# Optimization experiments

Hardware: AMD Instinct MI355X
Metric: run time of the kernel (lower is better)

Reference implementation:

```python
import jax, jax.numpy as jnp
import numpy as np

B, L, H, E = 8, 1024, 8, 64
S = 1024
T = 1.0


def setup_inputs() -> dict:
    key = jax.random.key(0)
    kq, kk, kv = jax.random.split(key, 3)
    q = jax.random.normal(kq, (B, L, H, E), dtype=jnp.float32)
    k = jax.random.normal(kk, (B, S, H, E), dtype=jnp.float32)
    v = jax.random.normal(kv, (B, S, H, E), dtype=jnp.float32)
    attn_mask = jnp.zeros((1,), dtype=bool)  # unused by the module
    return {"q": q, "k": k, "v": v, "attn_mask": attn_mask}


def reference(q, k, v, attn_mask):
    # q: [B,L,H,E], k/v: [B,S,H,E]; attn_mask unused (matches torch source)
    Bq, Lq, Hq, Eq = q.shape
    xq = jnp.transpose(q, (0, 2, 3, 1))  # [B,H,E,L]
    xk = jnp.transpose(k, (0, 2, 3, 1))  # [B,H,E,S]
    xv = jnp.transpose(v, (0, 2, 3, 1))  # [B,H,E,S]
    qf = jnp.fft.rfft(xq, axis=-1, norm="ortho")  # [B,H,E,Lf]
    kf = jnp.fft.rfft(xk, axis=-1, norm="ortho")  # [B,H,E,Sf]
    vf = jnp.fft.rfft(xv, axis=-1, norm="ortho")  # [B,H,E,Sf]
    # complex cross-frequency scores, contracted over head dim E
    scores = jnp.einsum("bhex,bhey->bhxy", qf, jnp.conj(kf)) / jnp.sqrt(
        jnp.float32(Eq)
    )  # [B,H,Lf,Sf] complex
    # magnitude softmax -> real weights, promoted back to complex (zero imag)
    attn = jax.nn.softmax(jnp.abs(scores) / jnp.float32(T), axis=-1)
    attn = attn.astype(scores.dtype)
    outf = jnp.einsum("bhxy,bhey->bhex", attn, vf)  # [B,H,E,Lf] complex
    out = jnp.fft.irfft(outf, n=Lq, axis=-1, norm="ortho")  # [B,H,E,L] real
    return jnp.transpose(out, (0, 3, 1, 2))  # [B,L,H,E]
```

## Files before the change

### kernel.cpp

```cpp
#include <hip/hip_runtime.h>
#include <hip/hip_fp16.h>
#include <math.h>

#define BATCH 8
#define LSEQ  1024
#define NH    8
#define EDIM  64
#define LF    513
#define NBH   64
#define YP    576

typedef _Float16 f16;
typedef _Float16 f16x8 __attribute__((ext_vector_type(8)));
typedef float    f32x4 __attribute__((ext_vector_type(4)));
typedef unsigned int u32x4 __attribute__((ext_vector_type(4)));

__device__ __forceinline__ float2 cadd(float2 a, float2 b){return make_float2(a.x+b.x, a.y+b.y);}
__device__ __forceinline__ float2 csub(float2 a, float2 b){return make_float2(a.x-b.x, a.y-b.y);}
__device__ __forceinline__ float2 cmuls(float2 w, float2 y, float sign){
  float wr = w.x, wi = sign * w.y;
  return make_float2(y.x*wr - y.y*wi, y.x*wi + y.y*wr);
}

template<int ST>
__device__ __forceinline__ void r4stage(const float2* S, float2* D,
                                        const float2* __restrict__ tw,
                                        int bt, float sign) {
  const int s = 1 << (2*ST);
  const int q = bt & (s - 1);
  const int j1 = bt - q;
  float2 a0 = S[bt], a1 = S[bt+256], a2 = S[bt+512], a3 = S[bt+768];
  float2 b0 = cadd(a0,a2), b1 = csub(a0,a2);
  float2 b2 = cadd(a1,a3), b3 = csub(a1,a3);
  float2 y0 = cadd(b0,b2), y2 = csub(b0,b2);
  float2 ib3 = make_float2(-sign*b3.y, sign*b3.x);
  float2 y1 = cadd(b1, ib3), y3 = csub(b1, ib3);
  const int wb = 4*bt - 3*q;
  D[wb]       = y0;
  D[wb +   s] = cmuls(tw[j1],   y1, sign);
  D[wb + 2*s] = cmuls(tw[2*j1], y2, sign);
  D[wb + 3*s] = cmuls(tw[3*j1], y3, sign);
}

__device__ __forceinline__ void fft1024x2_r4(float2* fb0, float2* fb1,
                                             const float2* __restrict__ tw,
                                             int t, float sign) {
  const int off = (t >> 8) << 10;
  const int bt  = t & 255;
  r4stage<0>(fb0+off, fb1+off, tw, bt, sign); __syncthreads();
  r4stage<1>(fb1+off, fb0+off, tw, bt, sign); __syncthreads();
  r4stage<2>(fb0+off, fb1+off, tw, bt, sign); __syncthreads();
  r4stage<3>(fb1+off, fb0+off, tw, bt, sign); __syncthreads();
  r4stage<4>(fb0+off, fb1+off, tw, bt, sign); __syncthreads();
}

__global__ __launch_bounds__(512) void rfft_pack_kernel(
    const float* __restrict__ q, const float* __restrict__ k, const float* __restrict__ v,
    f16* __restrict__ qf, f16* __restrict__ kf, f16* __restrict__ vfT) {
  __shared__ float2 fb0[2048];
  __shared__ float2 fb1[2048];
  __shared__ float2 tw[768];
  const int t = threadIdx.x;
  const int equad = blockIdx.x;
  const int bh = blockIdx.y;
  const int tensor = blockIdx.z;
  const int b = bh >> 3, h = bh & 7;
  const int e0 = equad * 4;
  const float* src = (tensor == 0) ? q : ((tensor == 1) ? k : v);

  for (int i = t; i < 768; i += 512) {
    float sv, cv;
    __sincosf(6.2831853071795864769f * (float)i * (1.0f / 1024.0f), &sv, &cv);
    tw[i] = make_float2(cv, sv);
  }
  #pragma unroll
  for (int i = 0; i < 2; i++) {
    int l = t + i * 512;
    float4 vv = *(const float4*)(src + (((size_t)b * LSEQ + l) * NH + h) * EDIM + e0);
    fb0[l]        = make_float2(vv.x, vv.y);
    fb0[1024 + l] = make_float2(vv.z, vv.w);
  }
  __syncthreads();
  fft1024x2_r4(fb0, fb1, tw, t, -1.0f);

  #pragma unroll
  for (int i = 0; i < 2; i++) {
    int kk = t + i * 512;
    if (kk <= 512) {
      const float sc = 0.015625f;
      if (tensor < 2) {
        union { f16 hh[8]; u32x4 u; } pk;
        #pragma unroll
        for (int f = 0; f < 2; f++) {
          float2 z  = fb1[(f << 10) + kk];
          float2 zn = fb1[(f << 10) + ((1024 - kk) & 1023)];
          pk.hh[f*4+0] = (f16)(sc * (z.x + zn.x));
          pk.hh[f*4+1] = (f16)(sc * (z.y - zn.y));
          pk.hh[f*4+2] = (f16)(sc * (z.y + zn.y));
          pk.hh[f*4+3] = (f16)(sc * (zn.x - z.x));
        }
        f16* dst = (tensor == 0) ? qf : kf;
        *(u32x4*)(dst + ((size_t)bh * YP + kk) * 128 + e0 * 2) = pk.u;
      } else {
        #pragma unroll
        for (int f = 0; f < 2; f++) {
          float2 z  = fb1[(f << 10) + kk];
          float2 zn = fb1[(f << 10) + ((1024 - kk) & 1023)];
          size_t base = (size_t)bh * 128 + e0 * 2 + f * 4;
          vfT[(base + 0) * YP + kk] = (f16)(sc * (z.x + zn.x));
          vfT[(base + 1) * YP + kk] = (f16)(sc * (z.y - zn.y));
          vfT[(base + 2) * YP + kk] = (f16)(sc * (z.y + zn.y));
          vfT[(base + 3) * YP + kk] = (f16)(sc * (zn.x - z.x));
        }
      }
    }
  }
  if (tensor == 2 && t < 63) {
    int kk = 513 + t;
    #pragma unroll
    for (int j = 0; j < 8; j++)
      vfT[((size_t)bh * 128 + e0 * 2 + j) * YP + kk] = (f16)0.0f;
  }
}

__device__ __forceinline__ int pmidx(int row, int y) {
  return row * YP + (y ^ ((row & 7) << 3));
}

__global__ __launch_bounds__(256, 4) void fused_attn_kernel(
    const f16* __restrict__ qf, const f16* __restrict__ kf,
    const f16* __restrict__ vfT, float* __restrict__ of) {
  __shared__ f16 pm[32 * YP];
  __shared__ float winv_s[32];
  const int tid = threadIdx.x;
  const int w = tid >> 6, l = tid & 63, lr = l & 15, lg = l >> 4;
  const int bh = blockIdx.y, x0 = blockIdx.x * 32;
  const int xsub = w & 1, yhalf = w >> 1;

  for (int i = tid; i < 2048; i += 256) {
    int row = i >> 6, yo = i & 63;
    if (yo) pm[pmidx(row, 512 + yo)] = (f16)0.0f;
  }

  const f16* qb = qf + ((size_t)bh * YP + x0 + xsub * 16 + lr) * 128 + lg * 8;
  f16x8 aq[4], aqs[4];
  #pragma unroll
  for (int c4 = 0; c4 < 4; c4++) {
    aq[c4] = *(const f16x8*)(qb + c4 * 32);
    u32x4 tt = *(const u32x4*)&aq[c4];
    u32x4 ss;
    #pragma unroll
    for (int d = 0; d < 4; d++)
      ss[d] = ((tt[d] >> 16) | (tt[d] << 16)) ^ 0x80000000u;
    aqs[c4] = *(const f16x8*)&ss;
  }

  const int ntile = yhalf ? 15 : 18;
  const f16* kb = kf + ((size_t)bh * YP + yhalf * 288 + lr) * 128 + lg * 8;

  f16x8 kA[4], kB[4];
  #pragma unroll
  for (int c4 = 0; c4 < 4; c4++) kA[c4] = *(const f16x8*)(kb + c4 * 32);

#define PROCA(KR, TT) {                                                        \
    f32x4 rr = {0.f,0.f,0.f,0.f}, ri = {0.f,0.f,0.f,0.f};                      \
    _Pragma("unroll")                                                          \
    for (int c4 = 0; c4 < 4; c4++) {                                           \
      rr = __builtin_amdgcn_mfma_f32_16x16x32_f16(aq[c4],  KR[c4], rr, 0,0,0); \
      ri = __builtin_amdgcn_mfma_f32_16x16x32_f16(aqs[c4], KR[c4], ri, 0,0,0); \
    }                                                                          \
    int y = yhalf * 288 + (TT) * 16 + lr;                                      \
    if (y <= 512) {                                                            \
      int rowb = xsub * 16 + lg * 4;                                           \
      _Pragma("unroll")                                                        \
      for (int i = 0; i < 4; i++)                                              \
        pm[pmidx(rowb + i, y)] = (f16)(0.125f * sqrtf(rr[i]*rr[i] + ri[i]*ri[i])); \
    }                                                                          \
  }

  for (int t = 0; t < ntile; t += 2) {
    if (t + 1 < ntile) {
      const f16* kp = kb + (size_t)(t + 1) * 2048;
      #pragma unroll
      for (int c4 = 0; c4 < 4; c4++) kB[c4] = *(const f16x8*)(kp + c4 * 32);
    }
    PROCA(kA, t)
    if (t + 1 < ntile) {
      if (t + 2 < ntile) {
        const f16* kp = kb + (size_t)(t + 2) * 2048;
        #pragma unroll
        for (int c4 = 0; c4 < 4; c4++) kA[c4] = *(const f16x8*)(kp + c4 * 32);
      }
      PROCA(kB, t + 1)
    }
  }
#undef PROCA
  __syncthreads();

  #pragma unroll 1
  for (int r = 0; r < 8; r++) {
    const int row = w * 8 + r;
    float mx = 0.0f;
    #pragma unroll
    for (int ps = 0; ps < 4; ps++) {
      __half2 hv = *(const __half2*)&pm[pmidx(row, 2 * (l + 64 * ps))];
      float2 f = __half22float2(hv);
      mx = fmaxf(mx, fmaxf(f.x, f.y));
    }
    if (l < 32) {
      __half2 hv = *(const __half2*)&pm[pmidx(row, 512 + 2 * l)];
      float2 f = __half22float2(hv);
      mx = fmaxf(mx, fmaxf(f.x, f.y));
    }
    #pragma unroll
    for (int o = 32; o > 0; o >>= 1) mx = fmaxf(mx, __shfl_xor(mx, o));

    float s = 0.0f;
    #pragma unroll
    for (int ps = 0; ps < 4; ps++) {
      int y = 2 * (l + 64 * ps);
      __half2 hv = *(const __half2*)&pm[pmidx(row, y)];
      float2 f = __half22float2(hv);
      float p0 = __expf(f.x - mx), p1 = __expf(f.y - mx);
      s += p0 + p1;
      *(__half2*)&pm[pmidx(row, y)] = __floats2half2_rn(p0, p1);
    }
    if (l < 32) {
      int y = 512 + 2 * l;
      __half2 hv = *(const __half2*)&pm[pmidx(row, y)];
      float2 f = __half22float2(hv);
      float p0 = (y <= 512) ? __expf(f.x - mx) : 0.0f;
      s += p0;
      *(__half2*)&pm[pmidx(row, y)] = __floats2half2_rn(p0, 0.0f);
    }
    #pragma unroll
    for (int o = 32; o > 0; o >>= 1) s += __shfl_xor(s, o);
    if (l == 0) winv_s[row] = 1.0f / s;
  }
  __syncthreads();

  const int ch = (w >> 1) * 64;
  f32x4 acc[4];
  #pragma unroll
  for (int nt = 0; nt < 4; nt++) acc[nt] = (f32x4){0.f,0.f,0.f,0.f};
  const f16* vb = vfT + ((size_t)bh * 128 + ch + lr) * YP + lg * 8;

  f16x8 vA[4], vB[4];
  #pragma unroll
  for (int nt = 0; nt < 4; nt++) vA[nt] = *(const f16x8*)(vb + (size_t)(nt * 16) * YP);

  for (int kc = 0; kc < 18; kc += 2) {
    #pragma unroll
    for (int nt = 0; nt < 4; nt++)
      vB[nt] = *(const f16x8*)(vb + (size_t)(nt * 16) * YP + (kc + 1) * 32);
    {
      f16x8 a = *(const f16x8*)&pm[pmidx(xsub * 16 + lr, kc * 32 + lg * 8)];
      #pragma unroll
      for (int nt = 0; nt < 4; nt++)
        acc[nt] = __builtin_amdgcn_mfma_f32_16x16x32_f16(a, vA[nt], acc[nt], 0, 0, 0);
    }
    if (kc + 2 < 18) {
      #pragma unroll
      for (int nt = 0; nt < 4; nt++)
        vA[nt] = *(const f16x8*)(vb + (size_t)(nt * 16) * YP + (kc + 2) * 32);
    }
    {
      f16x8 a = *(const f16x8*)&pm[pmidx(xsub * 16 + lr, (kc + 1) * 32 + lg * 8)];
      #pragma unroll
      for (int nt = 0; nt < 4; nt++)
        acc[nt] = __builtin_amdgcn_mfma_f32_16x16x32_f16(a, vB[nt], acc[nt], 0, 0, 0);
    }
  }
  #pragma unroll
  for (int i = 0; i < 4; i++) {
    int xl = xsub * 16 + lg * 4 + i;
    int x = x0 + xl;
    if (x < LF) {
      float wv = winv_s[xl];
      #pragma unroll
      for (int nt = 0; nt < 4; nt++)
        of[((size_t)bh * LF + x) * 128 + ch + nt * 16 + lr] = acc[nt][i] * wv;
    }
  }
}

__global__ __launch_bounds__(512) void irfft_kernel(
    const float* __restrict__ of, float* __restrict__ out) {
  __shared__ float2 fb0[2048];
  __shared__ float2 fb1[2048];
  __shared__ float2 tw[768];
  const int t = threadIdx.x;
  const int equad = blockIdx.x;
  const int bh = blockIdx.y;
  const int b = bh >> 3, h = bh & 7;
  const int e0 = equad * 4;

  for (int i = t; i < 768; i += 512) {
    float sv, cv;
    __sincosf(6.2831853071795864769f * (float)i * (1.0f / 1024.0f), &sv, &cv);
    tw[i] = make_float2(cv, sv);
  }
  #pragma unroll
  for (int i = 0; i < 2; i++) {
    int kk = t + i * 512;
    if (kk <= 512) {
      const float* pr = of + ((size_t)bh * LF + kk) * 128 + e0 * 2;
      float4 r0 = *(const float4*)pr;
      float4 r1 = *(const float4*)(pr + 4);
      fb0[kk]        = make_float2(r0.x - r0.w, r0.y + r0.z);
      fb0[1024 + kk] = make_float2(r1.x - r1.w, r1.y + r1.z);
      if (kk >= 1 && kk <= 511) {
        fb0[1024 - kk]        = make_float2(r0.x + r0.w, r0.z - r0.y);
        fb0[1024 + 1024 - kk] = make_float2(r1.x + r1.w, r1.z - r1.y);
      }
    }
  }
  __syncthreads();
  fft1024x2_r4(fb0, fb1, tw, t, +1.0f);
  #pragma unroll
  for (int i = 0; i < 2; i++) {
    int l = t + i * 512;
    float2 z0 = fb1[l], z1 = fb1[1024 + l];
    float4 o = make_float4(0.03125f * z0.x, 0.03125f * z0.y,
                           0.03125f * z1.x, 0.03125f * z1.y);
    *(float4*)(out + (((size_t)b * LSEQ + l) * NH + h) * EDIM + e0) = o;
  }
}

extern "C" void kernel_launch(void* const* d_in, const int* in_sizes, int n_in,
                              void* d_out, int out_size, void* d_ws, size_t ws_size,
                              hipStream_t stream) {
  const float* q = (const float*)d_in[0];
  const float* k = (const float*)d_in[1];
  const float* v = (const float*)d_in[2];
  float* out = (float*)d_out;
  char* ws = (char*)d_ws;

  f16*   qf  = (f16*)(ws);
  f16*   kf  = (f16*)(ws + 9437184);
  f16*   vfT = (f16*)(ws + 18874368);
  float* of  = (float*)(ws + 28311552);

  rfft_pack_kernel<<<dim3(16, NBH, 3), 512, 0, stream>>>(q, k, v, qf, kf, vfT);
  fused_attn_kernel<<<dim3(17, NBH), 256, 0, stream>>>(qf, kf, vfT, of);
  irfft_kernel<<<dim3(16, NBH), 512, 0, stream>>>(of, out);
}
```

Baseline: 262.5 us.

## Swizzle FFT shared-memory indices and shrink attention tile to 16 query rows

Applies an XOR swizzle to every shared-memory index in the radix-4 FFT stages of the forward and inverse FFT kernels, to reduce LDS bank conflicts from strided butterfly accesses. The fused attention kernel now handles 16 frequency rows per block instead of 32. The four waves split the key range four ways for the score computation and the 128 output channels four ways for the value product. This halves LDS use and doubles the grid size for more occupancy, but each K/V tile is reused across fewer query rows, raising global traffic, and the explicit register double-buffering of loads is removed.

```diff
diff --git a/kernel.cpp b/kernel.cpp
--- a/kernel.cpp
+++ b/kernel.cpp
@@ -21,6 +21,7 @@
   float wr = w.x, wi = sign * w.y;
   return make_float2(y.x*wr - y.y*wi, y.x*wi + y.y*wr);
 }
+__device__ __forceinline__ int SW(int i){ return i ^ ((i >> 4) & 15); }
 
 template<int ST>
 __device__ __forceinline__ void r4stage(const float2* S, float2* D,
@@ -29,17 +30,17 @@
   const int s = 1 << (2*ST);
   const int q = bt & (s - 1);
   const int j1 = bt - q;
-  float2 a0 = S[bt], a1 = S[bt+256], a2 = S[bt+512], a3 = S[bt+768];
+  float2 a0 = S[SW(bt)], a1 = S[SW(bt+256)], a2 = S[SW(bt+512)], a3 = S[SW(bt+768)];
   float2 b0 = cadd(a0,a2), b1 = csub(a0,a2);
   float2 b2 = cadd(a1,a3), b3 = csub(a1,a3);
   float2 y0 = cadd(b0,b2), y2 = csub(b0,b2);
   float2 ib3 = make_float2(-sign*b3.y, sign*b3.x);
   float2 y1 = cadd(b1, ib3), y3 = csub(b1, ib3);
   const int wb = 4*bt - 3*q;
-  D[wb]       = y0;
-  D[wb +   s] = cmuls(tw[j1],   y1, sign);
-  D[wb + 2*s] = cmuls(tw[2*j1], y2, sign);
-  D[wb + 3*s] = cmuls(tw[3*j1], y3, sign);
+  D[SW(wb)]       = y0;
+  D[SW(wb +   s)] = cmuls(tw[j1],   y1, sign);
+  D[SW(wb + 2*s)] = cmuls(tw[2*j1], y2, sign);
+  D[SW(wb + 3*s)] = cmuls(tw[3*j1], y3, sign);
 }
 
 __device__ __forceinline__ void fft1024x2_r4(float2* fb0, float2* fb1,
@@ -77,8 +78,8 @@
   for (int i = 0; i < 2; i++) {
     int l = t + i * 512;
     float4 vv = *(const float4*)(src + (((size_t)b * LSEQ + l) * NH + h) * EDIM + e0);
-    fb0[l]        = make_float2(vv.x, vv.y);
-    fb0[1024 + l] = make_float2(vv.z, vv.w);
+    fb0[SW(l)]        = make_float2(vv.x, vv.y);
+    fb0[1024 + SW(l)] = make_float2(vv.z, vv.w);
   }
   __syncthreads();
   fft1024x2_r4(fb0, fb1, tw, t, -1.0f);
@@ -87,13 +88,14 @@
   for (int i = 0; i < 2; i++) {
     int kk = t + i * 512;
     if (kk <= 512) {
+      const int kn = (1024 - kk) & 1023;
       const float sc = 0.015625f;
       if (tensor < 2) {
         union { f16 hh[8]; u32x4 u; } pk;
         #pragma unroll
         for (int f = 0; f < 2; f++) {
-          float2 z  = fb1[(f << 10) + kk];
-          float2 zn = fb1[(f << 10) + ((1024 - kk) & 1023)];
+          float2 z  = fb1[(f << 10) + SW(kk)];
+          float2 zn = fb1[(f << 10) + SW(kn)];
           pk.hh[f*4+0] = (f16)(sc * (z.x + zn.x));
           pk.hh[f*4+1] = (f16)(sc * (z.y - zn.y));
           pk.hh[f*4+2] = (f16)(sc * (z.y + zn.y));
@@ -104,8 +106,8 @@
       } else {
         #pragma unroll
         for (int f = 0; f < 2; f++) {
-          float2 z  = fb1[(f << 10) + kk];
-          float2 zn = fb1[(f << 10) + ((1024 - kk) & 1023)];
+          float2 z  = fb1[(f << 10) + SW(kk)];
+          float2 zn = fb1[(f << 10) + SW(kn)];
           size_t base = (size_t)bh * 128 + e0 * 2 + f * 4;
           vfT[(base + 0) * YP + kk] = (f16)(sc * (z.x + zn.x));
           vfT[(base + 1) * YP + kk] = (f16)(sc * (z.y - zn.y));
@@ -127,22 +129,21 @@
   return row * YP + (y ^ ((row & 7) << 3));
 }
 
-__global__ __launch_bounds__(256, 4) void fused_attn_kernel(
+__global__ __launch_bounds__(256, 6) void fused_attn_kernel(
     const f16* __restrict__ qf, const f16* __restrict__ kf,
     const f16* __restrict__ vfT, float* __restrict__ of) {
-  __shared__ f16 pm[32 * YP];
-  __shared__ float winv_s[32];
+  __shared__ f16 pm[16 * YP];
+  __shared__ float winv_s[16];
   const int tid = threadIdx.x;
   const int w = tid >> 6, l = tid & 63, lr = l & 15, lg = l >> 4;
-  const int bh = blockIdx.y, x0 = blockIdx.x * 32;
-  const int xsub = w & 1, yhalf = w >> 1;
-
-  for (int i = tid; i < 2048; i += 256) {
+  const int bh = blockIdx.y, x0 = blockIdx.x * 16;
+
+  for (int i = tid; i < 1024; i += 256) {
     int row = i >> 6, yo = i & 63;
     if (yo) pm[pmidx(row, 512 + yo)] = (f16)0.0f;
   }
 
-  const f16* qb = qf + ((size_t)bh * YP + x0 + xsub * 16 + lr) * 128 + lg * 8;
+  const f16* qb = qf + ((size_t)bh * YP + x0 + lr) * 128 + lg * 8;
   f16x8 aq[4], aqs[4];
   #pragma unroll
   for (int c4 = 0; c4 < 4; c4++) {
@@ -155,51 +156,32 @@
     aqs[c4] = *(const f16x8*)&ss;
   }
 
-  const int ntile = yhalf ? 15 : 18;
-  const f16* kb = kf + ((size_t)bh * YP + yhalf * 288 + lr) * 128 + lg * 8;
-
-  f16x8 kA[4], kB[4];
-  #pragma unroll
-  for (int c4 = 0; c4 < 4; c4++) kA[c4] = *(const f16x8*)(kb + c4 * 32);
-
-#define PROCA(KR, TT) {                                                        \
-    f32x4 rr = {0.f,0.f,0.f,0.f}, ri = {0.f,0.f,0.f,0.f};                      \
-    _Pragma("unroll")                                                          \
-    for (int c4 = 0; c4 < 4; c4++) {                                           \
-      rr = __builtin_amdgcn_mfma_f32_16x16x32_f16(aq[c4],  KR[c4], rr, 0,0,0); \
-      ri = __builtin_amdgcn_mfma_f32_16x16x32_f16(aqs[c4], KR[c4], ri, 0,0,0); \
-    }                                                                          \
-    int y = yhalf * 288 + (TT) * 16 + lr;                                      \
-    if (y <= 512) {                                                            \
-      int rowb = xsub * 16 + lg * 4;                                           \
-      _Pragma("unroll")                                                        \
-      for (int i = 0; i < 4; i++)                                              \
-        pm[pmidx(rowb + i, y)] = (f16)(0.125f * sqrtf(rr[i]*rr[i] + ri[i]*ri[i])); \
-    }                                                                          \
-  }
-
-  for (int t = 0; t < ntile; t += 2) {
-    if (t + 1 < ntile) {
-      const f16* kp = kb + (size_t)(t + 1) * 2048;
+  const int ntile = (w == 3) ? 6 : 9;
+  const f16* kb = kf + ((size_t)bh * YP + w * 144 + lr) * 128 + lg * 8;
+  for (int t = 0; t < ntile; t++) {
+    f16x8 bk[4];
+    #pragma unroll
+    for (int c4 = 0; c4 < 4; c4++)
+      bk[c4] = *(const f16x8*)(kb + (size_t)t * 2048 + c4 * 32);
+    f32x4 rr = {0.f,0.f,0.f,0.f}, ri = {0.f,0.f,0.f,0.f};
+    #pragma unroll
+    for (int c4 = 0; c4 < 4; c4++) {
+      rr = __builtin_amdgcn_mfma_f32_16x16x32_f16(aq[c4],  bk[c4], rr, 0, 0, 0);
+      ri = __builtin_amdgcn_mfma_f32_16x16x32_f16(aqs[c4], bk[c4], ri, 0, 0, 0);
+    }
+    int y = w * 144 + t * 16 + lr;
+    if (y <= 512) {
+      int rowb = lg * 4;
       #pragma unroll
-      for (int c4 = 0; c4 < 4; c4++) kB[c4] = *(const f16x8*)(kp + c4 * 32);
-    }
-    PROCA(kA, t)
-    if (t + 1 < ntile) {
-      if (t + 2 < ntile) {
-        const f16* kp = kb + (size_t)(t + 2) * 2048;
-        #pragma unroll
-        for (int c4 = 0; c4 < 4; c4++) kA[c4] = *(const f16x8*)(kp + c4 * 32);
-      }
-      PROCA(kB, t + 1)
-    }
-  }
-#undef PROCA
+      for (int i = 0; i < 4; i++)
+        pm[pmidx(rowb + i, y)] = (f16)(0.125f * sqrtf(rr[i]*rr[i] + ri[i]*ri[i]));
+    }
+  }
   __syncthreads();
 
   #pragma unroll 1
-  for (int r = 0; r < 8; r++) {
-    const int row = w * 8 + r;
+  for (int r = 0; r < 4; r++) {
+    const int row = w * 4 + r;
     float mx = 0.0f;
     #pragma unroll
     for (int ps = 0; ps < 4; ps++) {
@@ -239,46 +221,27 @@
   }
   __syncthreads();
 
-  const int ch = (w >> 1) * 64;
-  f32x4 acc[4];
-  #pragma unroll
-  for (int nt = 0; nt < 4; nt++) acc[nt] = (f32x4){0.f,0.f,0.f,0.f};
+  const int ch = w * 32;
+  f32x4 acc[2];
+  #pragma unroll
+  for (int nt = 0; nt < 2; nt++) acc[nt] = (f32x4){0.f,0.f,0.f,0.f};
   const f16* vb = vfT + ((size_t)bh * 128 + ch + lr) * YP + lg * 8;
-
-  f16x8 vA[4], vB[4];
-  #pragma unroll
-  for (int nt = 0; nt < 4; nt++) vA[nt] = *(const f16x8*)(vb + (size_t)(nt * 16) * YP);
-
-  for (int kc = 0; kc < 18; kc += 2) {
-    #pragma unroll
-    for (int nt = 0; nt < 4; nt++)
-      vB[nt] = *(const f16x8*)(vb + (size_t)(nt * 16) * YP + (kc + 1) * 32);
-    {
-      f16x8 a = *(const f16x8*)&pm[pmidx(xsub * 16 + lr, kc * 32 + lg * 8)];
-      #pragma unroll
-      for (int nt = 0; nt < 4; nt++)
-        acc[nt] = __builtin_amdgcn_mfma_f32_16x16x32_f16(a, vA[nt], acc[nt], 0, 0, 0);
-    }
-    if (kc + 2 < 18) {
-      #pragma unroll
-      for (int nt = 0; nt < 4; nt++)
-        vA[nt] = *(const f16x8*)(vb + (size_t)(nt * 16) * YP + (kc + 2) * 32);
-    }
-    {
-      f16x8 a = *(const f16x8*)&pm[pmidx(xsub * 16 + lr, (kc + 1) * 32 + lg * 8)];
-      #pragma unroll
-      for (int nt = 0; nt < 4; nt++)
-        acc[nt] = __builtin_amdgcn_mfma_f32_16x16x32_f16(a, vB[nt], acc[nt], 0, 0, 0);
+  for (int kc = 0; kc < 18; kc++) {
+    f16x8 a = *(const f16x8*)&pm[pmidx(lr, kc * 32 + lg * 8)];
+    #pragma unroll
+    for (int nt = 0; nt < 2; nt++) {
+      f16x8 b = *(const f16x8*)(vb + (size_t)(nt * 16) * YP + kc * 32);
+      acc[nt] = __builtin_amdgcn_mfma_f32_16x16x32_f16(a, b, acc[nt], 0, 0, 0);
     }
   }
   #pragma unroll
   for (int i = 0; i < 4; i++) {
-    int xl = xsub * 16 + lg * 4 + i;
+    int xl = lg * 4 + i;
     int x = x0 + xl;
     if (x < LF) {
       float wv = winv_s[xl];
       #pragma unroll
-      for (int nt = 0; nt < 4; nt++)
+      for (int nt = 0; nt < 2; nt++)
         of[((size_t)bh * LF + x) * 128 + ch + nt * 16 + lr] = acc[nt][i] * wv;
     }
   }
@@ -307,11 +270,11 @@
       const float* pr = of + ((size_t)bh * LF + kk) * 128 + e0 * 2;
       float4 r0 = *(const float4*)pr;
       float4 r1 = *(const float4*)(pr + 4);
-      fb0[kk]        = make_float2(r0.x - r0.w, r0.y + r0.z);
-      fb0[1024 + kk] = make_float2(r1.x - r1.w, r1.y + r1.z);
+      fb0[SW(kk)]        = make_float2(r0.x - r0.w, r0.y + r0.z);
+      fb0[1024 + SW(kk)] = make_float2(r1.x - r1.w, r1.y + r1.z);
       if (kk >= 1 && kk <= 511) {
-        fb0[1024 - kk]        = make_float2(r0.x + r0.w, r0.z - r0.y);
-        fb0[1024 + 1024 - kk] = make_float2(r1.x + r1.w, r1.z - r1.y);
+        fb0[SW(1024 - kk)]        = make_float2(r0.x + r0.w, r0.z - r0.y);
+        fb0[1024 + SW(1024 - kk)] = make_float2(r1.x + r1.w, r1.z - r1.y);
       }
     }
   }
@@ -320,7 +283,7 @@
   #pragma unroll
   for (int i = 0; i < 2; i++) {
     int l = t + i * 512;
-    float2 z0 = fb1[l], z1 = fb1[1024 + l];
+    float2 z0 = fb1[SW(l)], z1 = fb1[1024 + SW(l)];
     float4 o = make_float4(0.03125f * z0.x, 0.03125f * z0.y,
                            0.03125f * z1.x, 0.03125f * z1.y);
     *(float4*)(out + (((size_t)b * LSEQ + l) * NH + h) * EDIM + e0) = o;
@@ -342,6 +305,6 @@
   float* of  = (float*)(ws + 28311552);
 
   rfft_pack_kernel<<<dim3(16, NBH, 3), 512, 0, stream>>>(q, k, v, qf, kf, vfT);
-  fused_attn_kernel<<<dim3(17, NBH), 256, 0, stream>>>(qf, kf, vfT, of);
+  fused_attn_kernel<<<dim3(33, NBH), 256, 0, stream>>>(qf, kf, vfT, of);
   irfft_kernel<<<dim3(16, NBH), 512, 0, stream>>>(of, out);
 }
```

Result: faster. 250.2 us (-4.7%).
